# Kernel optimization log

Hardware: AMD Instinct MI355X
Metric: run time of the kernel (lower is better)

The kernel has to match this reference:

```python
import jax, jax.numpy as jnp
import numpy as np

EMB = 1024
HEADS = 16

def setup_inputs() -> dict:
    key = jax.random.key(0)
    ks = jax.random.split(key, 9)
    s = 1.0 / np.sqrt(EMB)
    x = jax.random.normal(ks[0], (2, 2048, EMB), dtype=jnp.float32)
    Wq = jax.random.normal(ks[1], (EMB, EMB), dtype=jnp.float32) * s
    bq = jax.random.normal(ks[2], (EMB,), dtype=jnp.float32) * s
    Wk = jax.random.normal(ks[3], (EMB, EMB), dtype=jnp.float32) * s
    bk = jax.random.normal(ks[4], (EMB,), dtype=jnp.float32) * s
    Wv = jax.random.normal(ks[5], (EMB, EMB), dtype=jnp.float32) * s
    bv = jax.random.normal(ks[6], (EMB,), dtype=jnp.float32) * s
    Wo = jax.random.normal(ks[7], (EMB, EMB), dtype=jnp.float32) * s
    bo = jax.random.normal(ks[8], (EMB,), dtype=jnp.float32) * s
    return {"x": x, "Wq": Wq, "bq": bq, "Wk": Wk, "bk": bk, "Wv": Wv, "bv": bv, "Wo": Wo, "bo": bo}

def reference(x, Wq, bq, Wk, bk, Wv, bv, Wo, bo):
    B, N, E = x.shape
    H = HEADS
    D = E // H
    # q/k/v projections, split heads: b n (h d) -> b h n d
    def proj(W, b):
        y = jnp.einsum('bne,ef->bnf', x, W.T) + b
        return y.reshape(B, N, H, D).transpose(0, 2, 1, 3)
    q = proj(Wq, bq)
    k = proj(Wk, bk)
    v = proj(Wv, bv)
    energy = jnp.einsum('bhqd,bhkd->bhqk', q, k)
    scaling = jnp.asarray(E, x.dtype) ** 0.5  # note: sqrt(emb_size), as in source
    att = jax.nn.softmax(energy / scaling, axis=-1)
    out = jnp.einsum('bhqk,bhkd->bhqd', att, v)
    out = out.transpose(0, 2, 1, 3).reshape(B, N, E)  # b h n d -> b n (h d)
    return jnp.einsum('bne,ef->bnf', out, Wo.T) + bo
```

## Files before the change

kernel.cpp:

```cpp
#include <hip/hip_runtime.h>
#include <hip/hip_bf16.h>
#include <stdint.h>

typedef __bf16 bf16;
typedef __bf16 bf16x8 __attribute__((ext_vector_type(8)));
typedef __bf16 bf16x4 __attribute__((ext_vector_type(4)));
typedef __bf16 bf16x2 __attribute__((ext_vector_type(2)));
typedef float  f32x4  __attribute__((ext_vector_type(4)));
typedef float  f32x16 __attribute__((ext_vector_type(16)));
typedef unsigned int uint;

#define MFMA(a,b,c)   __builtin_amdgcn_mfma_f32_16x16x32_bf16((a),(b),(c),0,0,0)
#define MFMA32(a,b,c) __builtin_amdgcn_mfma_f32_32x32x16_bf16((a),(b),(c),0,0,0)
#define EXP2(x)       __builtin_amdgcn_exp2f(x)

__device__ __forceinline__ void gload_lds16(const void* g, void* lds) {
  __builtin_amdgcn_global_load_lds(
      (const __attribute__((address_space(1))) uint32_t*)g,
      (__attribute__((address_space(3))) uint32_t*)lds, 16, 0, 0);
}

__device__ __forceinline__ uint pk_bf16(float lo, float hi) {
  bf16x2 v; v[0] = (bf16)lo; v[1] = (bf16)hi;
  return __builtin_bit_cast(uint, v);
}

__global__ __launch_bounds__(256) void k_cvt(
    const float* __restrict__ x,
    const float* __restrict__ wq, const float* __restrict__ wk,
    const float* __restrict__ wv, const float* __restrict__ wo,
    bf16* __restrict__ xb, bf16* __restrict__ wqb, bf16* __restrict__ wkb,
    bf16* __restrict__ wvb, bf16* __restrict__ wob)
{
  int r = blockIdx.y;
  const float* s; bf16* d; int n;
  switch (r) {
    case 0: s = x;  d = xb;  n = 4194304; break;
    case 1: s = wq; d = wqb; n = 1048576; break;
    case 2: s = wk; d = wkb; n = 1048576; break;
    case 3: s = wv; d = wvb; n = 1048576; break;
    default: s = wo; d = wob; n = 1048576; break;
  }
  int i = (blockIdx.x * 256 + threadIdx.x) * 8;
  if (i >= n) return;
  const float4* sp = (const float4*)(s + i);
  float4 a = sp[0], b = sp[1];
  bf16x8 o;
  o[0]=(bf16)a.x; o[1]=(bf16)a.y; o[2]=(bf16)a.z; o[3]=(bf16)a.w;
  o[4]=(bf16)b.x; o[5]=(bf16)b.y; o[6]=(bf16)b.z; o[7]=(bf16)b.w;
  *(bf16x8*)(d + i) = o;
}

__global__ __launch_bounds__(256) void k_gemm_qkv(
    const bf16* __restrict__ A,
    const bf16* __restrict__ Wq, const bf16* __restrict__ Wk, const bf16* __restrict__ Wv,
    const float* __restrict__ bq, const float* __restrict__ bk, const float* __restrict__ bv,
    bf16* __restrict__ Qw, bf16* __restrict__ Kw, bf16* __restrict__ Vtw)
{
  __shared__ __align__(16) char As[8192];
  __shared__ __align__(16) char Bs[8192];
  int tid = threadIdx.x;
  int wv4 = tid >> 6, l = tid & 63, lo = l & 15, hi = l >> 4;
  int mt = blockIdx.x;
  int ft = blockIdx.y;
  int wsel = ft >> 3;
  const bf16* W = (wsel == 0) ? Wq : (wsel == 1) ? Wk : Wv;
  const float* bias = (wsel == 0) ? bq : (wsel == 1) ? bk : bv;
  int f0 = (ft & 7) * 128;
  const bf16* Ab = A + (size_t)mt * 128 * 1024;
  const bf16* Wb = W + (size_t)f0 * 1024;
  int wm = wv4 >> 1, wf = wv4 & 1;
  f32x4 acc[4][4];
  #pragma unroll
  for (int i = 0; i < 4; i++)
    #pragma unroll
    for (int j = 0; j < 4; j++) acc[i][j] = (f32x4){0.f, 0.f, 0.f, 0.f};

  for (int k0 = 0; k0 < 1024; k0 += 32) {
    __syncthreads();
    #pragma unroll
    for (int p = 0; p < 2; p++) {
      int e = p * 256 + tid;
      int row = e >> 2, sl = e & 3;
      gload_lds16(Ab + row * 1024 + k0 + sl * 8, As + (p * 256 + wv4 * 64) * 16);
      gload_lds16(Wb + row * 1024 + k0 + sl * 8, Bs + (p * 256 + wv4 * 64) * 16);
    }
    __syncthreads();
    bf16x8 af[4], bfr[4];
    #pragma unroll
    for (int ms = 0; ms < 4; ms++)
      af[ms] = *(const bf16x8*)(As + ((wm * 64 + ms * 16 + lo) * 32 + hi * 8) * 2);
    #pragma unroll
    for (int fs = 0; fs < 4; fs++)
      bfr[fs] = *(const bf16x8*)(Bs + ((wf * 64 + fs * 16 + lo) * 32 + hi * 8) * 2);
    #pragma unroll
    for (int ms = 0; ms < 4; ms++)
      #pragma unroll
      for (int fs = 0; fs < 4; fs++)
        acc[ms][fs] = MFMA(af[ms], bfr[fs], acc[ms][fs]);
  }

  float bv4[4];
  #pragma unroll
  for (int fs = 0; fs < 4; fs++) bv4[fs] = bias[f0 + wf * 64 + fs * 16 + lo];
  #pragma unroll
  for (int ms = 0; ms < 4; ms++) {
    #pragma unroll
    for (int fs = 0; fs < 4; fs++) {
      int fl = f0 + wf * 64 + fs * 16 + lo;
      int h = fl >> 6, dd = fl & 63;
      #pragma unroll
      for (int r = 0; r < 4; r++) {
        int m = mt * 128 + wm * 64 + ms * 16 + hi * 4 + r;
        int b = m >> 11, n = m & 2047;
        float val = acc[ms][fs][r] + bv4[fs];
        if (wsel == 0)      Qw[(((size_t)(b * 16 + h) * 2048 + n) * 64) + dd] = (bf16)(val * 0.0450842199527801f);
        else if (wsel == 1) Kw[(((size_t)(b * 16 + h) * 2048 + n) * 64) + dd] = (bf16)val;
        else                Vtw[(((size_t)(b * 16 + h) * 64 + dd) * 2048) + n] = (bf16)val;
      }
    }
  }
}

__global__ __launch_bounds__(256, 2) void k_attn(
    const bf16* __restrict__ Q, const bf16* __restrict__ K,
    const bf16* __restrict__ Vt, bf16* __restrict__ O)
{
  __shared__ __align__(16) char Ks[2][8192];
  __shared__ __align__(16) char Vs[2][8192];
  int tid = threadIdx.x;
  int wid = tid >> 6, l = tid & 63;
  int lq = l & 31, hi1 = l >> 5;
  int qt = blockIdx.x, bh = blockIdx.y;
  int qg = qt * 128 + wid * 32 + lq;
  const bf16* Kb = K + (size_t)bh * 2048 * 64;
  const bf16* Vb = Vt + (size_t)bh * 64 * 2048;

  bf16x8 qf[4];
  const bf16* Qb = Q + ((size_t)bh * 2048 + qg) * 64 + hi1 * 8;
  #pragma unroll
  for (int c = 0; c < 4; c++) qf[c] = *(const bf16x8*)(Qb + 16 * c);

  f32x16 o0, o1, zz;
  #pragma unroll
  for (int r = 0; r < 16; r++) { zz[r] = 0.f; o0[r] = 0.f; o1[r] = 0.f; }
  float ls = 0.f;

  int srow = tid >> 3, slot = tid & 7;
  int swz = 16 * (slot ^ (srow & 7));
  int swk = lq & 7;
  uint4 k0r, k1r, v0r, v1r;
  #define STAGE(t) {                                                          \
    k0r = *(const uint4*)(Kb + (size_t)((t)*64 + srow) * 64 + slot * 8);      \
    k1r = *(const uint4*)(Kb + (size_t)((t)*64 + srow + 32) * 64 + slot * 8); \
    v0r = *(const uint4*)(Vb + (size_t)srow * 2048 + (t)*64 + slot * 8);      \
    v1r = *(const uint4*)(Vb + (size_t)(srow + 32) * 2048 + (t)*64 + slot * 8); }
  #define WRBUF(bi) {                                  \
    *(uint4*)(Ks[bi] + srow * 128 + swz)        = k0r; \
    *(uint4*)(Ks[bi] + (srow + 32) * 128 + swz) = k1r; \
    *(uint4*)(Vs[bi] + srow * 128 + swz)        = v0r; \
    *(uint4*)(Vs[bi] + (srow + 32) * 128 + swz) = v1r; }
  #define EXPSUM(S, T0, T1, T2, T3)                     \
    _Pragma("unroll")                                   \
    for (int r = 0; r < 16; r += 4) {                   \
      S[r]   = EXP2(S[r]);   T0 += S[r];                \
      S[r+1] = EXP2(S[r+1]); T1 += S[r+1];              \
      S[r+2] = EXP2(S[r+2]); T2 += S[r+2];              \
      S[r+3] = EXP2(S[r+3]); T3 += S[r+3];              \
    }
  #define PACK(dst, plo, phi)                                                \
    _Pragma("unroll")                                                        \
    for (int m = 0; m < 2; m++) {                                            \
      uint a0 = pk_bf16(plo[8*m+0], plo[8*m+1]);                             \
      uint b0 = pk_bf16(plo[8*m+4], plo[8*m+5]);                             \
      asm volatile("v_permlane32_swap_b32 %0, %1" : "+v"(a0), "+v"(b0));     \
      uint a1 = pk_bf16(plo[8*m+2], plo[8*m+3]);                             \
      uint b1 = pk_bf16(plo[8*m+6], plo[8*m+7]);                             \
      asm volatile("v_permlane32_swap_b32 %0, %1" : "+v"(a1), "+v"(b1));     \
      dst[m] = (uint4){a0, a1, b0, b1};                                      \
      uint c0 = pk_bf16(phi[8*m+0], phi[8*m+1]);                             \
      uint d0 = pk_bf16(phi[8*m+4], phi[8*m+5]);                             \
      asm volatile("v_permlane32_swap_b32 %0, %1" : "+v"(c0), "+v"(d0));     \
      uint c1 = pk_bf16(phi[8*m+2], phi[8*m+3]);                             \
      uint d1 = pk_bf16(phi[8*m+6], phi[8*m+7]);                             \
      asm volatile("v_permlane32_swap_b32 %0, %1" : "+v"(c1), "+v"(d1));     \
      dst[2+m] = (uint4){c0, c1, d0, d1};                                    \
    }

  STAGE(0);
  WRBUF(0);
  STAGE(1);

  for (int t = 0; t < 32; ++t) {
    __syncthreads();
    const char* Kc = Ks[t & 1];
    const char* Vc = Vs[t & 1];

    bf16x8 kf0[4], kf1[4];
    #pragma unroll
    for (int c = 0; c < 4; c++) {
      kf0[c] = *(const bf16x8*)(Kc + lq * 128 + 16 * ((2*c + hi1) ^ swk));
      kf1[c] = *(const bf16x8*)(Kc + (32 + lq) * 128 + 16 * ((2*c + hi1) ^ swk));
    }

    __builtin_amdgcn_s_setprio(1);
    f32x16 s0 = MFMA32(kf0[0], qf[0], zz);
    f32x16 s1 = MFMA32(kf1[0], qf[0], zz);
    #pragma unroll
    for (int c = 1; c < 4; c++) {
      s0 = MFMA32(kf0[c], qf[c], s0);
      s1 = MFMA32(kf1[c], qf[c], s1);
    }
    __builtin_amdgcn_s_setprio(0);

    float t0 = 0.f, t1 = 0.f, t2 = 0.f, t3 = 0.f;
    EXPSUM(s0, t0, t1, t2, t3);
    EXPSUM(s1, t0, t1, t2, t3);
    ls += (t0 + t1) + (t2 + t3);

    uint4 pf[4];
    PACK(pf, s0, s1);

    __builtin_amdgcn_s_setprio(1);
    #pragma unroll
    for (int c = 0; c < 4; c++) {
      bf16x8 pb = __builtin_bit_cast(bf16x8, pf[c]);
      bf16x8 vf0 = *(const bf16x8*)(Vc + lq * 128 + 16 * ((2*c + hi1) ^ swk));
      o0 = MFMA32(vf0, pb, o0);
      bf16x8 vf1 = *(const bf16x8*)(Vc + (32 + lq) * 128 + 16 * ((2*c + hi1) ^ swk));
      o1 = MFMA32(vf1, pb, o1);
    }
    __builtin_amdgcn_s_setprio(0);

    if (t < 31) {
      WRBUF((t + 1) & 1);
      if (t < 30) STAGE(t + 2);
    }
  }
  #undef STAGE
  #undef WRBUF

  float lsum = ls + __shfl_xor(ls, 32);
  float inv = 1.0f / lsum;
  int b = bh >> 4, h = bh & 15;
  bf16* Ob = O + ((size_t)(b * 2048 + qg)) * 1024 + h * 64 + hi1 * 4;
  #pragma unroll
  for (int g = 0; g < 4; g++) {
    bf16x4 w0, w1;
    #pragma unroll
    for (int j = 0; j < 4; j++) {
      w0[j] = (bf16)(o0[4*g+j] * inv);
      w1[j] = (bf16)(o1[4*g+j] * inv);
    }
    *(bf16x4*)(Ob + g * 8)      = w0;
    *(bf16x4*)(Ob + 32 + g * 8) = w1;
  }
}

__global__ __launch_bounds__(256) void k_gemm_out(
    const bf16* __restrict__ A,
    const bf16* __restrict__ W,
    const float* __restrict__ bias,
    float* __restrict__ Cout)
{
  __shared__ __align__(16) char As[8192];
  __shared__ __align__(16) char Bs[8192];
  int tid = threadIdx.x;
  int wv4 = tid >> 6, l = tid & 63, lo = l & 15, hi = l >> 4;
  int mt = blockIdx.x;
  int f0 = blockIdx.y * 128;
  const bf16* Ab = A + (size_t)mt * 128 * 1024;
  const bf16* Wb = W + (size_t)f0 * 1024;
  int wm = wv4 >> 1, wf = wv4 & 1;
  f32x4 acc[4][4];
  #pragma unroll
  for (int i = 0; i < 4; i++)
    #pragma unroll
    for (int j = 0; j < 4; j++) acc[i][j] = (f32x4){0.f, 0.f, 0.f, 0.f};

  for (int k0 = 0; k0 < 1024; k0 += 32) {
    __syncthreads();
    #pragma unroll
    for (int p = 0; p < 2; p++) {
      int e = p * 256 + tid;
      int row = e >> 2, sl = e & 3;
      gload_lds16(Ab + row * 1024 + k0 + sl * 8, As + (p * 256 + wv4 * 64) * 16);
      gload_lds16(Wb + row * 1024 + k0 + sl * 8, Bs + (p * 256 + wv4 * 64) * 16);
    }
    __syncthreads();
    bf16x8 af[4], bfr[4];
    #pragma unroll
    for (int ms = 0; ms < 4; ms++)
      af[ms] = *(const bf16x8*)(As + ((wm * 64 + ms * 16 + lo) * 32 + hi * 8) * 2);
    #pragma unroll
    for (int fs = 0; fs < 4; fs++)
      bfr[fs] = *(const bf16x8*)(Bs + ((wf * 64 + fs * 16 + lo) * 32 + hi * 8) * 2);
    #pragma unroll
    for (int ms = 0; ms < 4; ms++)
      #pragma unroll
      for (int fs = 0; fs < 4; fs++)
        acc[ms][fs] = MFMA(af[ms], bfr[fs], acc[ms][fs]);
  }

  float bv4[4];
  #pragma unroll
  for (int fs = 0; fs < 4; fs++) bv4[fs] = bias[f0 + wf * 64 + fs * 16 + lo];
  #pragma unroll
  for (int ms = 0; ms < 4; ms++)
    #pragma unroll
    for (int fs = 0; fs < 4; fs++) {
      int f = f0 + wf * 64 + fs * 16 + lo;
      #pragma unroll
      for (int r = 0; r < 4; r++) {
        int m = mt * 128 + wm * 64 + ms * 16 + hi * 4 + r;
        Cout[(size_t)m * 1024 + f] = acc[ms][fs][r] + bv4[fs];
      }
    }
}

extern "C" void kernel_launch(void* const* d_in, const int* in_sizes, int n_in,
                              void* d_out, int out_size, void* d_ws, size_t ws_size,
                              hipStream_t stream) {
  const float* x  = (const float*)d_in[0];
  const float* Wq = (const float*)d_in[1];
  const float* bq = (const float*)d_in[2];
  const float* Wk = (const float*)d_in[3];
  const float* bk = (const float*)d_in[4];
  const float* Wv = (const float*)d_in[5];
  const float* bv = (const float*)d_in[6];
  const float* Wo = (const float*)d_in[7];
  const float* bo = (const float*)d_in[8];
  float* out = (float*)d_out;
  char* ws = (char*)d_ws;

  bf16* xb  = (bf16*)(ws);
  bf16* wqb = (bf16*)(ws + 8388608);
  bf16* wkb = (bf16*)(ws + 10485760);
  bf16* wvb = (bf16*)(ws + 12582912);
  bf16* wob = (bf16*)(ws + 14680064);
  bf16* Qw  = (bf16*)(ws + 16777216);
  bf16* Kw  = (bf16*)(ws + 25165824);
  bf16* Vtw = (bf16*)(ws + 33554432);
  bf16* Ow  = (bf16*)(ws + 41943040);

  k_cvt<<<dim3(2048, 5), 256, 0, stream>>>(x, Wq, Wk, Wv, Wo, xb, wqb, wkb, wvb, wob);
  k_gemm_qkv<<<dim3(32, 24), 256, 0, stream>>>(xb, wqb, wkb, wvb, bq, bk, bv, Qw, Kw, Vtw);
  k_attn<<<dim3(16, 32), 256, 0, stream>>>(Qw, Kw, Vtw, Ow);
  k_gemm_out<<<dim3(32, 8), 256, 0, stream>>>(Ow, wob, bo, out);
}
```

Baseline: 116.6 us.

## Double-buffer LDS with XOR swizzle in QKV and output GEMMs, 512 threads for out

```diff
diff --git a/kernel.cpp b/kernel.cpp
--- a/kernel.cpp
+++ b/kernel.cpp
@@ -51,14 +51,14 @@
   *(bf16x8*)(d + i) = o;
 }
 
-__global__ __launch_bounds__(256) void k_gemm_qkv(
+__global__ __launch_bounds__(256, 1) void k_gemm_qkv(
     const bf16* __restrict__ A,
     const bf16* __restrict__ Wq, const bf16* __restrict__ Wk, const bf16* __restrict__ Wv,
     const float* __restrict__ bq, const float* __restrict__ bk, const float* __restrict__ bv,
     bf16* __restrict__ Qw, bf16* __restrict__ Kw, bf16* __restrict__ Vtw)
 {
-  __shared__ __align__(16) char As[8192];
-  __shared__ __align__(16) char Bs[8192];
+  __shared__ __align__(16) char As[2][16384];
+  __shared__ __align__(16) char Bs[2][16384];
   int tid = threadIdx.x;
   int wv4 = tid >> 6, l = tid & 63, lo = l & 15, hi = l >> 4;
   int mt = blockIdx.x;
@@ -76,29 +76,46 @@
     #pragma unroll
     for (int j = 0; j < 4; j++) acc[i][j] = (f32x4){0.f, 0.f, 0.f, 0.f};
 
-  for (int k0 = 0; k0 < 1024; k0 += 32) {
+  #define STAGEG(t, bi) {                                              \
+    int k0 = (t) * 64;                                                 \
+    _Pragma("unroll")                                                  \
+    for (int p = 0; p < 4; p++) {                                      \
+      int sp = p * 256 + tid;                                          \
+      int row = sp >> 3, s = sp & 7;                                   \
+      int gc = k0 + 8 * (s ^ (row & 7));                               \
+      gload_lds16(Ab + (size_t)row * 1024 + gc, As[bi] + sp * 16);     \
+      gload_lds16(Wb + (size_t)row * 1024 + gc, Bs[bi] + sp * 16);     \
+    } }
+
+  STAGEG(0, 0);
+  for (int t = 0; t < 16; ++t) {
     __syncthreads();
-    #pragma unroll
-    for (int p = 0; p < 2; p++) {
-      int e = p * 256 + tid;
-      int row = e >> 2, sl = e & 3;
-      gload_lds16(Ab + row * 1024 + k0 + sl * 8, As + (p * 256 + wv4 * 64) * 16);
-      gload_lds16(Wb + row * 1024 + k0 + sl * 8, Bs + (p * 256 + wv4 * 64) * 16);
-    }
-    __syncthreads();
-    bf16x8 af[4], bfr[4];
-    #pragma unroll
-    for (int ms = 0; ms < 4; ms++)
-      af[ms] = *(const bf16x8*)(As + ((wm * 64 + ms * 16 + lo) * 32 + hi * 8) * 2);
-    #pragma unroll
-    for (int fs = 0; fs < 4; fs++)
-      bfr[fs] = *(const bf16x8*)(Bs + ((wf * 64 + fs * 16 + lo) * 32 + hi * 8) * 2);
-    #pragma unroll
-    for (int ms = 0; ms < 4; ms++)
-      #pragma unroll
-      for (int fs = 0; fs < 4; fs++)
-        acc[ms][fs] = MFMA(af[ms], bfr[fs], acc[ms][fs]);
-  }
+    if (t < 15) STAGEG(t + 1, (t + 1) & 1);
+    const char* Ac = As[t & 1];
+    const char* Bc = Bs[t & 1];
+    #pragma unroll
+    for (int kk = 0; kk < 2; kk++) {
+      bf16x8 af[4], bfr[4];
+      #pragma unroll
+      for (int ms = 0; ms < 4; ms++) {
+        int row = wm * 64 + ms * 16 + lo;
+        af[ms] = *(const bf16x8*)(Ac + row * 128 + 16 * ((kk * 4 + hi) ^ (row & 7)));
+      }
+      #pragma unroll
+      for (int fs = 0; fs < 4; fs++) {
+        int row = wf * 64 + fs * 16 + lo;
+        bfr[fs] = *(const bf16x8*)(Bc + row * 128 + 16 * ((kk * 4 + hi) ^ (row & 7)));
+      }
+      __builtin_amdgcn_s_setprio(1);
+      #pragma unroll
+      for (int ms = 0; ms < 4; ms++)
+        #pragma unroll
+        for (int fs = 0; fs < 4; fs++)
+          acc[ms][fs] = MFMA(af[ms], bfr[fs], acc[ms][fs]);
+      __builtin_amdgcn_s_setprio(0);
+    }
+  }
+  #undef STAGEG
 
   float bv4[4];
   #pragma unroll
@@ -257,63 +274,80 @@
   }
 }
 
-__global__ __launch_bounds__(256) void k_gemm_out(
+__global__ __launch_bounds__(512, 1) void k_gemm_out(
     const bf16* __restrict__ A,
     const bf16* __restrict__ W,
     const float* __restrict__ bias,
     float* __restrict__ Cout)
 {
-  __shared__ __align__(16) char As[8192];
-  __shared__ __align__(16) char Bs[8192];
+  __shared__ __align__(16) char As[2][16384];
+  __shared__ __align__(16) char Bs[2][16384];
   int tid = threadIdx.x;
-  int wv4 = tid >> 6, l = tid & 63, lo = l & 15, hi = l >> 4;
+  int wid = tid >> 6, l = tid & 63, lo = l & 15, hi = l >> 4;
   int mt = blockIdx.x;
   int f0 = blockIdx.y * 128;
   const bf16* Ab = A + (size_t)mt * 128 * 1024;
   const bf16* Wb = W + (size_t)f0 * 1024;
-  int wm = wv4 >> 1, wf = wv4 & 1;
-  f32x4 acc[4][4];
+  int wm = wid >> 2, wf = wid & 3;
+  f32x4 acc[4][2];
   #pragma unroll
   for (int i = 0; i < 4; i++)
     #pragma unroll
-    for (int j = 0; j < 4; j++) acc[i][j] = (f32x4){0.f, 0.f, 0.f, 0.f};
-
-  for (int k0 = 0; k0 < 1024; k0 += 32) {
+    for (int j = 0; j < 2; j++) acc[i][j] = (f32x4){0.f, 0.f, 0.f, 0.f};
+
+  #define STAGEG(t, bi) {                                              \
+    int k0 = (t) * 64;                                                 \
+    _Pragma("unroll")                                                  \
+    for (int p = 0; p < 2; p++) {                                      \
+      int sp = p * 512 + tid;                                          \
+      int row = sp >> 3, s = sp & 7;                                   \
+      int gc = k0 + 8 * (s ^ (row & 7));                               \
+      gload_lds16(Ab + (size_t)row * 1024 + gc, As[bi] + sp * 16);     \
+      gload_lds16(Wb + (size_t)row * 1024 + gc, Bs[bi] + sp * 16);     \
+    } }
+
+  STAGEG(0, 0);
+  for (int t = 0; t < 16; ++t) {
     __syncthreads();
-    #pragma unroll
-    for (int p = 0; p < 2; p++) {
-      int e = p * 256 + tid;
-      int row = e >> 2, sl = e & 3;
-      gload_lds16(Ab + row * 1024 + k0 + sl * 8, As + (p * 256 + wv4 * 64) * 16);
-      gload_lds16(Wb + row * 1024 + k0 + sl * 8, Bs + (p * 256 + wv4 * 64) * 16);
-    }
-    __syncthreads();
-    bf16x8 af[4], bfr[4];
-    #pragma unroll
-    for (int ms = 0; ms < 4; ms++)
-      af[ms] = *(const bf16x8*)(As + ((wm * 64 + ms * 16 + lo) * 32 + hi * 8) * 2);
-    #pragma unroll
-    for (int fs = 0; fs < 4; fs++)
-      bfr[fs] = *(const bf16x8*)(Bs + ((wf * 64 + fs * 16 + lo) * 32 + hi * 8) * 2);
-    #pragma unroll
-    for (int ms = 0; ms < 4; ms++)
-      #pragma unroll
-      for (int fs = 0; fs < 4; fs++)
-        acc[ms][fs] = MFMA(af[ms], bfr[fs], acc[ms][fs]);
-  }
-
-  float bv4[4];
-  #pragma unroll
-  for (int fs = 0; fs < 4; fs++) bv4[fs] = bias[f0 + wf * 64 + fs * 16 + lo];
+    if (t < 15) STAGEG(t + 1, (t + 1) & 1);
+    const char* Ac = As[t & 1];
+    const char* Bc = Bs[t & 1];
+    #pragma unroll
+    for (int kk = 0; kk < 2; kk++) {
+      bf16x8 af[4], bfr[2];
+      #pragma unroll
+      for (int ms = 0; ms < 4; ms++) {
+        int row = wm * 64 + ms * 16 + lo;
+        af[ms] = *(const bf16x8*)(Ac + row * 128 + 16 * ((kk * 4 + hi) ^ (row & 7)));
+      }
+      #pragma unroll
+      for (int fs = 0; fs < 2; fs++) {
+        int row = wf * 32 + fs * 16 + lo;
+        bfr[fs] = *(const bf16x8*)(Bc + row * 128 + 16 * ((kk * 4 + hi) ^ (row & 7)));
+      }
+      __builtin_amdgcn_s_setprio(1);
+      #pragma unroll
+      for (int ms = 0; ms < 4; ms++)
+        #pragma unroll
+        for (int fs = 0; fs < 2; fs++)
+          acc[ms][fs] = MFMA(af[ms], bfr[fs], acc[ms][fs]);
+      __builtin_amdgcn_s_setprio(0);
+    }
+  }
+  #undef STAGEG
+
+  float bv2[2];
+  #pragma unroll
+  for (int fs = 0; fs < 2; fs++) bv2[fs] = bias[f0 + wf * 32 + fs * 16 + lo];
   #pragma unroll
   for (int ms = 0; ms < 4; ms++)
     #pragma unroll
-    for (int fs = 0; fs < 4; fs++) {
-      int f = f0 + wf * 64 + fs * 16 + lo;
+    for (int fs = 0; fs < 2; fs++) {
+      int f = f0 + wf * 32 + fs * 16 + lo;
       #pragma unroll
       for (int r = 0; r < 4; r++) {
         int m = mt * 128 + wm * 64 + ms * 16 + hi * 4 + r;
-        Cout[(size_t)m * 1024 + f] = acc[ms][fs][r] + bv4[fs];
+        Cout[(size_t)m * 1024 + f] = acc[ms][fs][r] + bv2[fs];
       }
     }
 }
@@ -346,5 +380,5 @@
   k_cvt<<<dim3(2048, 5), 256, 0, stream>>>(x, Wq, Wk, Wv, Wo, xb, wqb, wkb, wvb, wob);
   k_gemm_qkv<<<dim3(32, 24), 256, 0, stream>>>(xb, wqb, wkb, wvb, bq, bk, bv, Qw, Kw, Vtw);
   k_attn<<<dim3(16, 32), 256, 0, stream>>>(Qw, Kw, Vtw, Ow);
-  k_gemm_out<<<dim3(32, 8), 256, 0, stream>>>(Ow, wob, bo, out);
-}
+  k_gemm_out<<<dim3(32, 8), 512, 0, stream>>>(Ow, wob, bo, out);
+}
```

Result: no change. 118.8 us (+1.9%).
